# Optimization experiments

Hardware: AMD Instinct MI355X
Metric: run time of the kernel (lower is better)

Reference implementation:

```python
import jax, jax.numpy as jnp
import numpy as np

QN, QP = -8.0, 7.0  # int4: Qn=-2**3, Qp=2**3-1
LOG2E = 1.4426950408889634  # 1/ln(2)

def round_ste(x):
    return x + jax.lax.stop_gradient(jnp.round(x) - x)

def sg(x):
    return jax.lax.stop_gradient(x)

def mean_var_int(x_int, scale=1024):
    """Serial integer running-mean/var recurrence over the last dim.
    x_int: (B,H,N,D) int32. Returns mu (int values, float32) and varn float32, shape (B,H,N,1).
    Matches the torch loop: m_i = m_{i-1} + (x_i-m_{i-1})*int(1024/(i+1))//1024,
    v_i = v_{i-1} + (x_i-m_{i-1})*(x_i-m_i), with m_0=x_0, v_0=0 (same as the general
    recurrence with m_{-1}=v_{-1}=0 since int(1024/1)=1024)."""
    D = x_int.shape[3]
    coef = jnp.array([scale // (i + 1) for i in range(D)], dtype=jnp.int32)
    xt = jnp.moveaxis(x_int, 3, 0)  # (D,B,H,N)
    z = jnp.zeros(x_int.shape[:3], jnp.int32)
    def step(carry, inp):
        m, v = carry
        xi, c = inp
        d = xi - m
        new_m = m + (d * c) // scale  # floor division, matches torch //
        new_v = v + d * (xi - new_m)
        return (new_m, new_v), None
    (m, v), _ = jax.lax.scan(step, (z, z), (xt, coef))
    mu = m[..., None].astype(jnp.float32)
    varn = v[..., None].astype(jnp.float32) / D
    return mu, varn

def q_attention_forward(x0, qkv_w, qkv_b, qkv_alpha, qkv_act_alpha,
                        proj_w, proj_b, proj_alpha, proj_act_alpha,
                        norm_q_w, norm_q_b, norm_k_w, norm_k_b,
                        q_alpha, k_alpha, v_alpha, attn_alpha,
                        num_heads=12):
    B, N, C = x0.shape
    H = num_heads
    hd = C // H
    head_scale = hd ** -0.5

    # input activation quantization (ActQ_v2 then .int())
    a_in = qkv_act_alpha.mean()
    x0_2b = sg(jnp.round(jnp.clip(x0 / a_in, QN, QP)))  # int-valued (B,N,C)

    # int4 qkv weight quantization (per-output-channel alpha), integer GEMM
    w_qkv = sg(jnp.round(jnp.clip(qkv_w / qkv_alpha[:, None], QN, QP)))  # (3C,C)
    qkv = jnp.einsum('bnc,oc->bno', x0_2b, w_qkv)
    bias_i = sg(jnp.trunc(qkv_b / a_in / qkv_alpha))  # bias.int()
    qkv = qkv + bias_i

    qkv = jnp.transpose(qkv.reshape(B, N, 3, H, hd), (2, 0, 3, 1, 4))
    q0, k0, v0 = qkv[0], qkv[1], qkv[2]  # (B,H,N,hd)
    alpha_r = qkv_alpha.reshape(3, H, 1, hd)

    # q branch: scaled integer mean/var norm + scaled quantization
    xq = q0 * alpha_r[0]
    mu_q, var_q = mean_var_int(xq.astype(jnp.int32))
    q1 = (xq - mu_q) / (jnp.sqrt(var_q) + 1e-5)
    aq = q_alpha.mean()
    q2 = sg(jnp.round(jnp.clip((q1 + norm_q_b / norm_q_w) * norm_q_w / aq, QN, QP)))

    # k branch
    xk = k0 * alpha_r[1]
    mu_k, var_k = mean_var_int(xk.astype(jnp.int32))
    k1 = (xk - mu_k) / (jnp.sqrt(var_k) + 1e-5)
    ak = k_alpha.mean()
    k2 = sg(jnp.round(jnp.clip((k1 + norm_k_b / norm_k_w) * norm_k_w / ak, QN, QP)))

    # v branch
    av = v_alpha.mean()
    v2 = sg(jnp.round(jnp.clip(v0 * (a_in * alpha_r[2]) / av, QN, QP)))

    # integer q @ k^T
    qk = jnp.einsum('bhqd,bhkd->bhqk', q2, k2)  # (B,H,N,N)

    # power-of-two softmax approximation: 2^floor(e) * (1 + frac(e))
    s = head_scale * aq * ak
    e = LOG2E * s * qk
    f = jnp.floor(e)
    attn_exp = jnp.exp2(f) * (1.0 + (e - f))
    am = attn_alpha.mean()
    attn_norm = attn_exp / attn_exp.sum(-1, keepdims=True)
    attn2 = sg(jnp.round(jnp.clip(attn_norm / am, QN, QP)))

    x1p = jnp.einsum('bhqk,bhkd->bhqd', attn2, v2)
    x1p = jnp.transpose(x1p, (0, 2, 1, 3)).reshape(B, N, C)

    # proj-act quantization (round_pass STE, no .int() here in torch)
    ap = proj_act_alpha.mean()
    x1_2b = round_ste(jnp.clip(x1p * (am * av) / ap, QN, QP))

    w_p = sg(jnp.round(jnp.clip(proj_w / proj_alpha[:, None], QN, QP)))  # w_q.int()
    x2 = jnp.einsum('bnc,oc->bno', x1_2b, w_p) * proj_alpha * ap + proj_b
    return x2

def setup_inputs() -> dict:
    key = jax.random.key(0)
    ks = jax.random.split(key, 17)
    B, N, C, H = 4, 1024, 768, 12
    u = lambda k, shape, lo, hi: jax.random.uniform(k, shape, jnp.float32, lo, hi)
    return {
        "x0": jax.random.normal(ks[0], (B, N, C), jnp.float32),
        "qkv_w": jax.random.normal(ks[1], (3 * C, C), jnp.float32) * 0.02,
        "qkv_b": jax.random.normal(ks[2], (3 * C,), jnp.float32),
        "qkv_alpha": u(ks[3], (3 * C,), 0.008, 0.012),
        "qkv_act_alpha": u(ks[4], (C,), 0.25, 0.35),
        "proj_w": jax.random.normal(ks[5], (C, C), jnp.float32) * 0.02,
        "proj_b": jax.random.normal(ks[6], (C,), jnp.float32) * 0.02,
        "proj_alpha": u(ks[7], (C,), 0.008, 0.012),
        "proj_act_alpha": u(ks[8], (C,), 0.008, 0.012),
        "norm_q_w": u(ks[9], (C // H,), 0.8, 1.2),
        "norm_q_b": jax.random.normal(ks[10], (C // H,), jnp.float32) * 0.1,
        "norm_k_w": u(ks[11], (C // H,), 0.8, 1.2),
        "norm_k_b": jax.random.normal(ks[12], (C // H,), jnp.float32) * 0.1,
        "q_alpha": u(ks[13], (H,), 0.25, 0.35),
        "k_alpha": u(ks[14], (H,), 0.25, 0.35),
        "v_alpha": u(ks[15], (H,), 0.15, 0.25),
        "attn_alpha": u(ks[16], (H,), 0.0008, 0.0015),
    }

def reference(x0, qkv_w, qkv_b, qkv_alpha, qkv_act_alpha,
              proj_w, proj_b, proj_alpha, proj_act_alpha,
              norm_q_w, norm_q_b, norm_k_w, norm_k_b,
              q_alpha, k_alpha, v_alpha, attn_alpha):
    return q_attention_forward(x0, qkv_w, qkv_b, qkv_alpha, qkv_act_alpha,
                               proj_w, proj_b, proj_alpha, proj_act_alpha,
                               norm_q_w, norm_q_b, norm_k_w, norm_k_b,
                               q_alpha, k_alpha, v_alpha, attn_alpha)
```

## Files before the change

### kernel.cpp

```cpp
#include <hip/hip_runtime.h>

typedef unsigned short u16;
typedef unsigned int u32;
typedef __attribute__((ext_vector_type(8))) u16 u16x8;
typedef __attribute__((ext_vector_type(8))) __bf16 bf16x8;
typedef __attribute__((ext_vector_type(4))) float f32x4;

#define LOG2E_F 1.4426950408889634f

__device__ __forceinline__ u16 f2bf(float f) {
  return (u16)(__float_as_uint(f) >> 16);
}
__device__ __forceinline__ float clip87(float x) {
  return fminf(fmaxf(x, -8.0f), 7.0f);
}

typedef const __attribute__((address_space(1))) u32* gp32;
typedef __attribute__((address_space(3))) u32* lp32;
__device__ __forceinline__ void gl16(const void* g, void* l) {
  __builtin_amdgcn_global_load_lds((gp32)g, (lp32)l, 16, 0, 0);
}

__global__ void k_scalars(const float* __restrict__ qkv_act_alpha,
                          const float* __restrict__ proj_act_alpha,
                          const float* __restrict__ q_alpha,
                          const float* __restrict__ k_alpha,
                          const float* __restrict__ v_alpha,
                          const float* __restrict__ attn_alpha,
                          float* __restrict__ scal) {
  int tid = threadIdx.x;
  int wave = tid >> 6, lane = tid & 63;
  if (wave < 6) {
    const float* src = nullptr; int n = 0;
    switch (wave) {
      case 0: src = qkv_act_alpha;  n = 768; break;
      case 1: src = q_alpha;        n = 12;  break;
      case 2: src = k_alpha;        n = 12;  break;
      case 3: src = v_alpha;        n = 12;  break;
      case 4: src = attn_alpha;     n = 12;  break;
      case 5: src = proj_act_alpha; n = 768; break;
    }
    double s = 0.0;
    for (int i = lane; i < n; i += 64) s += (double)src[i];
    s += __shfl_xor(s, 1);
    s += __shfl_xor(s, 2);
    s += __shfl_xor(s, 4);
    s += __shfl_xor(s, 8);
    s += __shfl_xor(s, 16);
    s += __shfl_xor(s, 32);
    if (lane == 0) scal[wave] = (float)(s / (double)n);
  }
  __syncthreads();
  if (tid == 0) {
    float aq = scal[1], ak = scal[2];
    float s_ = (0.125f * aq) * ak;
    scal[6] = LOG2E_F * s_;
    scal[7] = scal[4] * scal[3];
  }
}

__global__ __launch_bounds__(256) void k_quant_weights(
    const float* __restrict__ qkv_w, const float* __restrict__ qkv_alpha,
    const float* __restrict__ qkv_b, const float* __restrict__ proj_w,
    const float* __restrict__ proj_alpha, const float* __restrict__ scal,
    u16* __restrict__ wq, u16* __restrict__ wp, float* __restrict__ biasi) {
  int idx = blockIdx.x * 256 + threadIdx.x;
  const int T1 = 2304 * 768, T2 = 768 * 768;
  if (idx < T1) {
    int o = idx / 768;
    wq[idx] = f2bf(rintf(clip87(qkv_w[idx] / qkv_alpha[o])));
  } else if (idx < T1 + T2) {
    int j = idx - T1;
    int o = j / 768;
    wp[j] = f2bf(rintf(clip87(proj_w[j] / proj_alpha[o])));
  } else if (idx < T1 + T2 + 2304) {
    int o = idx - T1 - T2;
    biasi[o] = truncf((qkv_b[o] / scal[0]) / qkv_alpha[o]);
  }
}

__global__ __launch_bounds__(256) void k_quant_x0(const float* __restrict__ x0,
                                                  const float* __restrict__ scal,
                                                  u16* __restrict__ x0q) {
  int base = (blockIdx.x * 256 + threadIdx.x) * 8;
  float a = scal[0];
  f32x4 v0 = *(const f32x4*)&x0[base];
  f32x4 v1 = *(const f32x4*)&x0[base + 4];
  u16x8 o;
  #pragma unroll
  for (int j = 0; j < 4; j++) o[j] = f2bf(rintf(clip87(v0[j] / a)));
  #pragma unroll
  for (int j = 0; j < 4; j++) o[4 + j] = f2bf(rintf(clip87(v1[j] / a)));
  *(u16x8*)&x0q[base] = o;
}

#define BUF_A64(c) (smem_u16 + (c) * 4096)
#define BUF_B64(c) (smem_u16 + 8192 + (c) * 4096)

__device__ __forceinline__ void stage64(const u16* gAl, const u16* gBl, int K,
                                        u16* bufA, u16* bufB, int w) {
  gl16(gAl, bufA + (w * 16) * 64);
  gl16(gAl + (size_t)8 * K, bufA + (w * 16 + 8) * 64);
  gl16(gBl, bufB + (w * 16) * 64);
  gl16(gBl + (size_t)8 * K, bufB + (w * 16 + 8) * 64);
}

__device__ __forceinline__ void gemm64(const u16* __restrict__ A,
                                       const u16* __restrict__ Bt, int K,
                                       int m0, int n0, u16* smem_u16,
                                       int lane, int wave, f32x4 acc[2][2]) {
  int rsub = lane >> 3;
  int jsrc = (lane & 7) ^ rsub;
  const u16* gAl = A + (size_t)(m0 + wave * 16 + rsub) * K + jsrc * 8;
  const u16* gBl = Bt + (size_t)(n0 + wave * 16 + rsub) * K + jsrc * 8;

  int arow = (wave >> 1) * 32 + (lane & 15);
  int brow = (wave & 1) * 32 + (lane & 15);
  int nsteps = K / 64;

  stage64(gAl, gBl, K, BUF_A64(0), BUF_B64(0), wave);
  __syncthreads();
  for (int t = 0; t < nsteps; t++) {
    int cur = t & 1;
    if (t + 1 < nsteps)
      stage64(gAl + (t + 1) * 64, gBl + (t + 1) * 64, K,
              BUF_A64(cur ^ 1), BUF_B64(cur ^ 1), wave);
    const u16* bA = BUF_A64(cur);
    const u16* bB = BUF_B64(cur);
    #pragma unroll
    for (int kk = 0; kk < 2; kk++) {
      int jj = ((kk * 4 + (lane >> 4)) ^ (lane & 7)) * 8;
      bf16x8 af0 = *(const bf16x8*)&bA[arow * 64 + jj];
      bf16x8 af1 = *(const bf16x8*)&bA[(arow + 16) * 64 + jj];
      bf16x8 bf0 = *(const bf16x8*)&bB[brow * 64 + jj];
      bf16x8 bf1 = *(const bf16x8*)&bB[(brow + 16) * 64 + jj];
      acc[0][0] = __builtin_amdgcn_mfma_f32_16x16x32_bf16(af0, bf0, acc[0][0], 0, 0, 0);
      acc[0][1] = __builtin_amdgcn_mfma_f32_16x16x32_bf16(af0, bf1, acc[0][1], 0, 0, 0);
      acc[1][0] = __builtin_amdgcn_mfma_f32_16x16x32_bf16(af1, bf0, acc[1][0], 0, 0, 0);
      acc[1][1] = __builtin_amdgcn_mfma_f32_16x16x32_bf16(af1, bf1, acc[1][1], 0, 0, 0);
    }
    __syncthreads();
  }
}

__global__ __launch_bounds__(256) void k_gemm_qkv(
    const u16* __restrict__ A, const u16* __restrict__ Bt,
    const float* __restrict__ biasi, const float* __restrict__ qkv_alpha,
    const float* __restrict__ nqw, const float* __restrict__ nqb,
    const float* __restrict__ nkw, const float* __restrict__ nkb,
    const float* __restrict__ scal,
    u16* __restrict__ q2, u16* __restrict__ k2, u16* __restrict__ v2t) {
  const int K = 768;
  __shared__ __align__(16) char smem[32768];
  u16* smem_u16 = (u16*)smem;
  float* xt = (float*)smem;
  int tid = threadIdx.x;
  int lane = tid & 63, wave = tid >> 6;
  int wr = wave >> 1, wc = wave & 1;
  int m0 = blockIdx.y * 64, n0 = blockIdx.x * 64;

  f32x4 acc[2][2];
  #pragma unroll
  for (int mi = 0; mi < 2; mi++)
    #pragma unroll
    for (int ni = 0; ni < 2; ni++) acc[mi][ni] = (f32x4){0.f, 0.f, 0.f, 0.f};

  gemm64(A, Bt, K, m0, n0, smem_u16, lane, wave, acc);

  int lrow = (lane >> 4) * 4, lcol = lane & 15;
  #pragma unroll
  for (int mi = 0; mi < 2; mi++)
    #pragma unroll
    for (int ni = 0; ni < 2; ni++) {
      int c = wc * 32 + ni * 16 + lcol;
      float bs = biasi[n0 + c];
      #pragma unroll
      for (int rr = 0; rr < 4; rr++) {
        int r = wr * 32 + mi * 16 + lrow + rr;
        xt[r * 65 + c] = acc[mi][ni][rr] + bs;
      }
    }
  __syncthreads();

  int branch = blockIdx.x / 12, h = blockIdx.x % 12;
  int b = m0 >> 10, nb = m0 & 1023;
  if (branch == 2) {
    int d = tid & 63, qr = tid >> 6;
    float av = scal[3];
    float coefv = scal[0] * qkv_alpha[1536 + h * 64 + d];
    u16* dst = v2t + ((size_t)(b * 12 + h) * 64 + d) * 1024 + nb + qr * 16;
    #pragma unroll
    for (int g = 0; g < 2; g++) {
      u16x8 t8;
      #pragma unroll
      for (int j = 0; j < 8; j++) {
        float val = xt[(qr * 16 + g * 8 + j) * 65 + d];
        t8[j] = f2bf(rintf(clip87((val * coefv) / av)));
      }
      *(u16x8*)(dst + g * 8) = t8;
    }
  } else if (tid < 64) {
    int r = tid;
    const float* alph = qkv_alpha + branch * 768 + h * 64;
    const float* wv = branch == 0 ? nqw : nkw;
    const float* bv = branch == 0 ? nqb : nkb;
    float as = branch == 0 ? scal[1] : scal[2];
    float xq[64];
    #pragma unroll
    for (int d = 0; d < 64; d++) xq[d] = xt[r * 65 + d] * alph[d];
    int m = 0, v = 0;
    #pragma unroll
    for (int i = 0; i < 64; i++) {
      int xi = (int)xq[i];
      int dd = xi - m;
      m += (dd * (1024 / (i + 1))) >> 10;
      v += dd * (xi - m);
    }
    float muf = (float)m;
    float den = sqrtf((float)v * 0.015625f) + 1e-5f;
    u16* outp = (branch == 0 ? q2 : k2) + ((size_t)(b * 12 + h) * 1024 + nb + r) * 64;
    #pragma unroll
    for (int g = 0; g < 8; g++) {
      u16x8 t8;
      #pragma unroll
      for (int j = 0; j < 8; j++) {
        int d = g * 8 + j;
        float q1 = (xq[d] - muf) / den;
        float bw = bv[d] / wv[d];
        float t = (q1 + bw) * wv[d] / as;
        t8[j] = f2bf(rintf(clip87(t)));
      }
      *(u16x8*)(outp + g * 8) = t8;
    }
  }
}

__global__ __launch_bounds__(256) void k_gemm_proj(
    const u16* __restrict__ A, const u16* __restrict__ Bt,
    float* __restrict__ Cout, const float* __restrict__ palpha,
    const float* __restrict__ pbias, const float* __restrict__ scal) {
  const int K = 768, N = 768;
  __shared__ __align__(16) char smem[32768];
  u16* smem_u16 = (u16*)smem;
  int tid = threadIdx.x;
  int lane = tid & 63, wave = tid >> 6;
  int wr = wave >> 1, wc = wave & 1;
  int m0 = blockIdx.y * 64, n0 = blockIdx.x * 64;

  f32x4 acc[2][2];
  #pragma unroll
  for (int mi = 0; mi < 2; mi++)
    #pragma unroll
    for (int ni = 0; ni < 2; ni++) acc[mi][ni] = (f32x4){0.f, 0.f, 0.f, 0.f};

  gemm64(A, Bt, K, m0, n0, smem_u16, lane, wave, acc);

  int lrow = (lane >> 4) * 4, lcol = lane & 15;
  float ap = scal[5];
  #pragma unroll
  for (int mi = 0; mi < 2; mi++)
    #pragma unroll
    for (int ni = 0; ni < 2; ni++) {
      int col = n0 + wc * 32 + ni * 16 + lcol;
      float pa = palpha[col], pb = pbias[col];
      #pragma unroll
      for (int rr = 0; rr < 4; rr++) {
        int row = m0 + wr * 32 + mi * 16 + lrow + rr;
        Cout[(size_t)row * N + col] = (acc[mi][ni][rr] * pa) * ap + pb;
      }
    }
}

__global__ __launch_bounds__(256) void k_attn(
    const u16* __restrict__ q2, const u16* __restrict__ k2,
    const u16* __restrict__ v2t, const float* __restrict__ scal,
    u16* __restrict__ x1q) {
  __shared__ __align__(16) u16 lK[64 * 72];
  __shared__ __align__(16) u16 lV[64 * 72];
  __shared__ __align__(16) u16 lP[64 * 72];
  __shared__ float rs_lds[64];
  int tid = threadIdx.x, lane = tid & 63, wave = tid >> 6;
  int qt = blockIdx.x, bh = blockIdx.y;
  const float escale = scal[6], am = scal[4], am_av = scal[7], apc = scal[5];

  size_t qrow = (size_t)bh * 1024 + qt * 64 + wave * 16 + (lane & 15);
  bf16x8 qf0 = *(const bf16x8*)(q2 + qrow * 64 + (lane >> 4) * 8);
  bf16x8 qf1 = *(const bf16x8*)(q2 + qrow * 64 + 32 + (lane >> 4) * 8);

  const u16* k2b = k2 + (size_t)bh * 1024 * 64;
  const u16* v2b = v2t + (size_t)bh * 64 * 1024;
  int sr = tid >> 2, sc = (tid & 3) * 16;

  double rsum[4] = {0.0, 0.0, 0.0, 0.0};
  for (int kt = 0; kt < 16; kt++) {
    const u16* src = k2b + (size_t)(kt * 64 + sr) * 64 + sc;
    *(u16x8*)&lK[sr * 72 + sc]     = *(const u16x8*)src;
    *(u16x8*)&lK[sr * 72 + sc + 8] = *(const u16x8*)(src + 8);
    __syncthreads();
    float part[4] = {0.f, 0.f, 0.f, 0.f};
    #pragma unroll
    for (int ct = 0; ct < 4; ct++) {
      bf16x8 kf0 = *(const bf16x8*)&lK[(ct * 16 + (lane & 15)) * 72 + (lane >> 4) * 8];
      bf16x8 kf1 = *(const bf16x8*)&lK[(ct * 16 + (lane & 15)) * 72 + 32 + (lane >> 4) * 8];
      f32x4 s = {0.f, 0.f, 0.f, 0.f};
      s = __builtin_amdgcn_mfma_f32_16x16x32_bf16(qf0, kf0, s, 0, 0, 0);
      s = __builtin_amdgcn_mfma_f32_16x16x32_bf16(qf1, kf1, s, 0, 0, 0);
      #pragma unroll
      for (int rr = 0; rr < 4; rr++) {
        float e = escale * s[rr];
        float f = floorf(e);
        float pe = ldexpf(1.0f + (e - f), (int)f);
        part[rr] += pe;
      }
    }
    #pragma unroll
    for (int rr = 0; rr < 4; rr++) rsum[rr] += (double)part[rr];
    __syncthreads();
  }
  #pragma unroll
  for (int rr = 0; rr < 4; rr++) {
    double s = rsum[rr];
    s += __shfl_xor(s, 1);
    s += __shfl_xor(s, 2);
    s += __shfl_xor(s, 4);
    s += __shfl_xor(s, 8);
    if ((lane & 15) == 0) rs_lds[wave * 16 + (lane >> 4) * 4 + rr] = (float)s;
  }
  __syncthreads();
  float fac[4];
  #pragma unroll
  for (int rr = 0; rr < 4; rr++)
    fac[rr] = 1.0f / (rs_lds[wave * 16 + (lane >> 4) * 4 + rr] * am);

  f32x4 accv[4];
  #pragma unroll
  for (int ct = 0; ct < 4; ct++) accv[ct] = (f32x4){0.f, 0.f, 0.f, 0.f};

  for (int kt = 0; kt < 16; kt++) {
    const u16* srcK = k2b + (size_t)(kt * 64 + sr) * 64 + sc;
    *(u16x8*)&lK[sr * 72 + sc]     = *(const u16x8*)srcK;
    *(u16x8*)&lK[sr * 72 + sc + 8] = *(const u16x8*)(srcK + 8);
    const u16* srcV = v2b + (size_t)sr * 1024 + kt * 64 + sc;
    *(u16x8*)&lV[sr * 72 + sc]     = *(const u16x8*)srcV;
    *(u16x8*)&lV[sr * 72 + sc + 8] = *(const u16x8*)(srcV + 8);
    __syncthreads();
    #pragma unroll
    for (int ct = 0; ct < 4; ct++) {
      bf16x8 kf0 = *(const bf16x8*)&lK[(ct * 16 + (lane & 15)) * 72 + (lane >> 4) * 8];
      bf16x8 kf1 = *(const bf16x8*)&lK[(ct * 16 + (lane & 15)) * 72 + 32 + (lane >> 4) * 8];
      f32x4 s = {0.f, 0.f, 0.f, 0.f};
      s = __builtin_amdgcn_mfma_f32_16x16x32_bf16(qf0, kf0, s, 0, 0, 0);
      s = __builtin_amdgcn_mfma_f32_16x16x32_bf16(qf1, kf1, s, 0, 0, 0);
      #pragma unroll
      for (int rr = 0; rr < 4; rr++) {
        float e = escale * s[rr];
        float f = floorf(e);
        float pe = ldexpf(1.0f + (e - f), (int)f);
        float a2 = rintf(fminf(pe * fac[rr], 7.0f));
        lP[(wave * 16 + (lane >> 4) * 4 + rr) * 72 + ct * 16 + (lane & 15)] = f2bf(a2);
      }
    }
    __syncthreads();
    bf16x8 pf0 = *(const bf16x8*)&lP[(wave * 16 + (lane & 15)) * 72 + (lane >> 4) * 8];
    bf16x8 pf1 = *(const bf16x8*)&lP[(wave * 16 + (lane & 15)) * 72 + 32 + (lane >> 4) * 8];
    #pragma unroll
    for (int ct = 0; ct < 4; ct++) {
      bf16x8 vf0 = *(const bf16x8*)&lV[(ct * 16 + (lane & 15)) * 72 + (lane >> 4) * 8];
      bf16x8 vf1 = *(const bf16x8*)&lV[(ct * 16 + (lane & 15)) * 72 + 32 + (lane >> 4) * 8];
      accv[ct] = __builtin_amdgcn_mfma_f32_16x16x32_bf16(pf0, vf0, accv[ct], 0, 0, 0);
      accv[ct] = __builtin_amdgcn_mfma_f32_16x16x32_bf16(pf1, vf1, accv[ct], 0, 0, 0);
    }
    __syncthreads();
  }

  int b = bh / 12, h = bh % 12;
  #pragma unroll
  for (int ct = 0; ct < 4; ct++)
    #pragma unroll
    for (int rr = 0; rr < 4; rr++) {
      int qr = qt * 64 + wave * 16 + (lane >> 4) * 4 + rr;
      int col = h * 64 + ct * 16 + (lane & 15);
      float t = (accv[ct][rr] * am_av) / apc;
      x1q[((size_t)b * 1024 + qr) * 768 + col] = f2bf(rintf(clip87(t)));
    }
}

extern "C" void kernel_launch(void* const* d_in, const int* in_sizes, int n_in,
                              void* d_out, int out_size, void* d_ws, size_t ws_size,
                              hipStream_t stream) {
  const float* x0             = (const float*)d_in[0];
  const float* qkv_w          = (const float*)d_in[1];
  const float* qkv_b          = (const float*)d_in[2];
  const float* qkv_alpha      = (const float*)d_in[3];
  const float* qkv_act_alpha  = (const float*)d_in[4];
  const float* proj_w         = (const float*)d_in[5];
  const float* proj_b         = (const float*)d_in[6];
  const float* proj_alpha     = (const float*)d_in[7];
  const float* proj_act_alpha = (const float*)d_in[8];
  const float* nqw            = (const float*)d_in[9];
  const float* nqb            = (const float*)d_in[10];
  const float* nkw            = (const float*)d_in[11];
  const float* nkb            = (const float*)d_in[12];
  const float* q_alpha        = (const float*)d_in[13];
  const float* k_alpha        = (const float*)d_in[14];
  const float* v_alpha        = (const float*)d_in[15];
  const float* attn_alpha     = (const float*)d_in[16];
  float* out = (float*)d_out;

  char* ws = (char*)d_ws;
  size_t off = 0;
  auto alloc = [&](size_t bytes) -> void* {
    off = (off + 255) & ~(size_t)255;
    void* p = ws + off;
    off += bytes;
    return p;
  };
  float* scal = (float*)alloc(64);
  u16* wq     = (u16*)alloc((size_t)2304 * 768 * 2);
  u16* wp     = (u16*)alloc((size_t)768 * 768 * 2);
  float* biasi= (float*)alloc((size_t)2304 * 4);
  u16* x0q    = (u16*)alloc((size_t)4096 * 768 * 2);
  u16* q2     = (u16*)alloc((size_t)48 * 1024 * 64 * 2);
  u16* k2     = (u16*)alloc((size_t)48 * 1024 * 64 * 2);
  u16* v2t    = (u16*)alloc((size_t)48 * 1024 * 64 * 2);
  u16* x1q    = (u16*)alloc((size_t)4096 * 768 * 2);

  k_scalars<<<1, 384, 0, stream>>>(qkv_act_alpha, proj_act_alpha, q_alpha, k_alpha,
                                   v_alpha, attn_alpha, scal);

  int totW = 2304 * 768 + 768 * 768 + 2304;
  k_quant_weights<<<(totW + 255) / 256, 256, 0, stream>>>(qkv_w, qkv_alpha, qkv_b,
                                                          proj_w, proj_alpha, scal,
                                                          wq, wp, biasi);

  k_quant_x0<<<(4096 * 768) / (256 * 8), 256, 0, stream>>>(x0, scal, x0q);

  k_gemm_qkv<<<dim3(36, 64), 256, 0, stream>>>(x0q, wq, biasi, qkv_alpha,
                                               nqw, nqb, nkw, nkb, scal,
                                               q2, k2, v2t);

  k_attn<<<dim3(16, 48), 256, 0, stream>>>(q2, k2, v2t, scal, x1q);

  k_gemm_proj<<<dim3(12, 64), 256, 0, stream>>>(x1q, wp, out, proj_alpha, proj_b, scal);
}
```

Measured before the change: 217.6 us.

## Double-buffer K/V tiles in attention and remap blocks across XCDs

The attention kernel now keeps two LDS buffers for K and V. The next tile's global loads are issued into registers before the current tile's compute, and written to LDS afterward, so load latency overlaps with MFMA and exp work. The block index is also remapped so consecutive workgroups spread across the 8 XCDs, aiming at better L2 locality for shared K/V per head. LDS use roughly doubles for K/V, which could lower occupancy, and the remap hardcodes 768 blocks.

```diff
diff --git a/kernel.cpp b/kernel.cpp
--- a/kernel.cpp
+++ b/kernel.cpp
@@ -275,12 +275,14 @@
     const u16* __restrict__ q2, const u16* __restrict__ k2,
     const u16* __restrict__ v2t, const float* __restrict__ scal,
     u16* __restrict__ x1q) {
-  __shared__ __align__(16) u16 lK[64 * 72];
-  __shared__ __align__(16) u16 lV[64 * 72];
+  __shared__ __align__(16) u16 lK[2][64 * 72];
+  __shared__ __align__(16) u16 lV[2][64 * 72];
   __shared__ __align__(16) u16 lP[64 * 72];
   __shared__ float rs_lds[64];
   int tid = threadIdx.x, lane = tid & 63, wave = tid >> 6;
-  int qt = blockIdx.x, bh = blockIdx.y;
+  int flat = blockIdx.y * gridDim.x + blockIdx.x;
+  int wg = (flat & 7) * 96 + (flat >> 3);
+  int qt = wg & 15, bh = wg >> 4;
   const float escale = scal[6], am = scal[4], am_av = scal[7], apc = scal[5];
 
   size_t qrow = (size_t)bh * 1024 + qt * 64 + wave * 16 + (lane & 15);
@@ -290,18 +292,29 @@
   const u16* k2b = k2 + (size_t)bh * 1024 * 64;
   const u16* v2b = v2t + (size_t)bh * 64 * 1024;
   int sr = tid >> 2, sc = (tid & 3) * 16;
+  int lofs = sr * 72 + sc;
 
   double rsum[4] = {0.0, 0.0, 0.0, 0.0};
+  {
+    const u16* s0 = k2b + (size_t)sr * 64 + sc;
+    u16x8 ka = *(const u16x8*)s0, kb = *(const u16x8*)(s0 + 8);
+    *(u16x8*)&lK[0][lofs] = ka;
+    *(u16x8*)&lK[0][lofs + 8] = kb;
+    __syncthreads();
+  }
+  int cur = 0;
   for (int kt = 0; kt < 16; kt++) {
-    const u16* src = k2b + (size_t)(kt * 64 + sr) * 64 + sc;
-    *(u16x8*)&lK[sr * 72 + sc]     = *(const u16x8*)src;
-    *(u16x8*)&lK[sr * 72 + sc + 8] = *(const u16x8*)(src + 8);
-    __syncthreads();
+    u16x8 ka, kb;
+    if (kt < 15) {
+      const u16* s1 = k2b + (size_t)((kt + 1) * 64 + sr) * 64 + sc;
+      ka = *(const u16x8*)s1; kb = *(const u16x8*)(s1 + 8);
+    }
+    const u16* lKc = lK[cur];
     float part[4] = {0.f, 0.f, 0.f, 0.f};
     #pragma unroll
     for (int ct = 0; ct < 4; ct++) {
-      bf16x8 kf0 = *(const bf16x8*)&lK[(ct * 16 + (lane & 15)) * 72 + (lane >> 4) * 8];
-      bf16x8 kf1 = *(const bf16x8*)&lK[(ct * 16 + (lane & 15)) * 72 + 32 + (lane >> 4) * 8];
+      bf16x8 kf0 = *(const bf16x8*)&lKc[(ct * 16 + (lane & 15)) * 72 + (lane >> 4) * 8];
+      bf16x8 kf1 = *(const bf16x8*)&lKc[(ct * 16 + (lane & 15)) * 72 + 32 + (lane >> 4) * 8];
       f32x4 s = {0.f, 0.f, 0.f, 0.f};
       s = __builtin_amdgcn_mfma_f32_16x16x32_bf16(qf0, kf0, s, 0, 0, 0);
       s = __builtin_amdgcn_mfma_f32_16x16x32_bf16(qf1, kf1, s, 0, 0, 0);
@@ -315,7 +328,12 @@
     }
     #pragma unroll
     for (int rr = 0; rr < 4; rr++) rsum[rr] += (double)part[rr];
-    __syncthreads();
+    if (kt < 15) {
+      *(u16x8*)&lK[cur ^ 1][lofs] = ka;
+      *(u16x8*)&lK[cur ^ 1][lofs + 8] = kb;
+    }
+    __syncthreads();
+    cur ^= 1;
   }
   #pragma unroll
   for (int rr = 0; rr < 4; rr++) {
@@ -336,18 +354,29 @@
   #pragma unroll
   for (int ct = 0; ct < 4; ct++) accv[ct] = (f32x4){0.f, 0.f, 0.f, 0.f};
 
+  {
+    const u16* sk = k2b + (size_t)sr * 64 + sc;
+    const u16* sv = v2b + (size_t)sr * 1024 + sc;
+    u16x8 ka = *(const u16x8*)sk, kb = *(const u16x8*)(sk + 8);
+    u16x8 va = *(const u16x8*)sv, vb = *(const u16x8*)(sv + 8);
+    *(u16x8*)&lK[0][lofs] = ka;  *(u16x8*)&lK[0][lofs + 8] = kb;
+    *(u16x8*)&lV[0][lofs] = va;  *(u16x8*)&lV[0][lofs + 8] = vb;
+    __syncthreads();
+  }
+  cur = 0;
   for (int kt = 0; kt < 16; kt++) {
-    const u16* srcK = k2b + (size_t)(kt * 64 + sr) * 64 + sc;
-    *(u16x8*)&lK[sr * 72 + sc]     = *(const u16x8*)srcK;
-    *(u16x8*)&lK[sr * 72 + sc + 8] = *(const u16x8*)(srcK + 8);
-    const u16* srcV = v2b + (size_t)sr * 1024 + kt * 64 + sc;
-    *(u16x8*)&lV[sr * 72 + sc]     = *(const u16x8*)srcV;
-    *(u16x8*)&lV[sr * 72 + sc + 8] = *(const u16x8*)(srcV + 8);
-    __syncthreads();
+    u16x8 ka, kb, va, vb;
+    if (kt < 15) {
+      const u16* sk = k2b + (size_t)((kt + 1) * 64 + sr) * 64 + sc;
+      const u16* sv = v2b + (size_t)sr * 1024 + (kt + 1) * 64 + sc;
+      ka = *(const u16x8*)sk; kb = *(const u16x8*)(sk + 8);
+      va = *(const u16x8*)sv; vb = *(const u16x8*)(sv + 8);
+    }
+    const u16* lKc = lK[cur];
     #pragma unroll
     for (int ct = 0; ct < 4; ct++) {
-      bf16x8 kf0 = *(const bf16x8*)&lK[(ct * 16 + (lane & 15)) * 72 + (lane >> 4) * 8];
-      bf16x8 kf1 = *(const bf16x8*)&lK[(ct * 16 + (lane & 15)) * 72 + 32 + (lane >> 4) * 8];
+      bf16x8 kf0 = *(const bf16x8*)&lKc[(ct * 16 + (lane & 15)) * 72 + (lane >> 4) * 8];
+      bf16x8 kf1 = *(const bf16x8*)&lKc[(ct * 16 + (lane & 15)) * 72 + 32 + (lane >> 4) * 8];
       f32x4 s = {0.f, 0.f, 0.f, 0.f};
       s = __builtin_amdgcn_mfma_f32_16x16x32_bf16(qf0, kf0, s, 0, 0, 0);
       s = __builtin_amdgcn_mfma_f32_16x16x32_bf16(qf1, kf1, s, 0, 0, 0);
@@ -360,17 +389,23 @@
         lP[(wave * 16 + (lane >> 4) * 4 + rr) * 72 + ct * 16 + (lane & 15)] = f2bf(a2);
       }
     }
-    __syncthreads();
+    if (kt < 15) {
+      *(u16x8*)&lK[cur ^ 1][lofs] = ka;  *(u16x8*)&lK[cur ^ 1][lofs + 8] = kb;
+      *(u16x8*)&lV[cur ^ 1][lofs] = va;  *(u16x8*)&lV[cur ^ 1][lofs + 8] = vb;
+    }
+    __syncthreads();
+    const u16* lVc = lV[cur];
     bf16x8 pf0 = *(const bf16x8*)&lP[(wave * 16 + (lane & 15)) * 72 + (lane >> 4) * 8];
     bf16x8 pf1 = *(const bf16x8*)&lP[(wave * 16 + (lane & 15)) * 72 + 32 + (lane >> 4) * 8];
     #pragma unroll
     for (int ct = 0; ct < 4; ct++) {
-      bf16x8 vf0 = *(const bf16x8*)&lV[(ct * 16 + (lane & 15)) * 72 + (lane >> 4) * 8];
-      bf16x8 vf1 = *(const bf16x8*)&lV[(ct * 16 + (lane & 15)) * 72 + 32 + (lane >> 4) * 8];
+      bf16x8 vf0 = *(const bf16x8*)&lVc[(ct * 16 + (lane & 15)) * 72 + (lane >> 4) * 8];
+      bf16x8 vf1 = *(const bf16x8*)&lVc[(ct * 16 + (lane & 15)) * 72 + 32 + (lane >> 4) * 8];
       accv[ct] = __builtin_amdgcn_mfma_f32_16x16x32_bf16(pf0, vf0, accv[ct], 0, 0, 0);
       accv[ct] = __builtin_amdgcn_mfma_f32_16x16x32_bf16(pf1, vf1, accv[ct], 0, 0, 0);
     }
     __syncthreads();
+    cur ^= 1;
   }
 
   int b = bh / 12, h = bh % 12;
```

New measurement: 209.4 us. 3.8% less time.
